# Kernel tuning notes

Hardware: AMD Instinct MI355X
Metric: run time of the kernel (lower is better)

The kernel has to match this reference:

```python
import jax, jax.numpy as jnp
import numpy as np

LAMBDA = 20.0
EPS = 1e-06
LAYER_WEIGHTS = (1.0, 0.5, 0.25, 0.125)


def _hungarian(cost):
    """Jonker-Volgenant shortest augmenting path LAP solver (same optimum as
    scipy.optimize.linear_sum_assignment). Returns col index per row."""
    cost = np.asarray(cost, dtype=np.float64)
    n = cost.shape[0]
    INF = 1e18
    u = np.zeros(n + 1)
    v = np.zeros(n + 1)
    p = np.zeros(n + 1, dtype=np.int64)   # p[j] = row matched to col j (1-indexed)
    way = np.zeros(n + 1, dtype=np.int64)
    for i in range(1, n + 1):
        p[0] = i
        j0 = 0
        minv = np.full(n + 1, INF)
        used = np.zeros(n + 1, dtype=bool)
        while True:
            used[j0] = True
            i0 = p[j0]
            free = np.nonzero(~used[1:])[0] + 1  # unused cols (1-indexed)
            cur = cost[i0 - 1, free - 1] - u[i0] - v[free]
            better = cur < minv[free]
            minv[free] = np.where(better, cur, minv[free])
            way[free] = np.where(better, j0, way[free])
            k = free[np.argmin(minv[free])]
            delta = minv[k]
            u[p[used]] += delta
            v[np.nonzero(used)[0]] -= delta
            minv[~used] -= delta
            j0 = k
            if p[j0] == 0:
                break
        while j0:
            j1 = way[j0]
            p[j0] = p[j1]
            j0 = j1
    col_of_row = np.zeros(n, dtype=np.int32)
    for j in range(1, n + 1):
        col_of_row[p[j] - 1] = j - 1
    return col_of_row


def _lap_cols(cost):
    n = cost.shape[0]
    return jax.pure_callback(
        lambda c: _hungarian(np.asarray(c)),
        jax.ShapeDtypeStruct((n,), np.int32),
        cost)


def _one_hot_matching(cols, n):
    return jnp.zeros((n, n), dtype=jnp.float32).at[jnp.arange(n), cols].set(1.0)


def _lap_solve_impl(cost):
    n = cost.shape[0]
    return _one_hot_matching(_lap_cols(cost), n)


@jax.custom_vjp
def lap_solve(cost):
    return _lap_solve_impl(cost)


def _lap_fwd(cost):
    lab = _lap_solve_impl(cost)
    return lab, (cost, lab)


def _lap_bwd(res, g):
    # Blackbox differentiation (Vlastelica et al.): re-solve on perturbed costs.
    cost, lab = res
    lab_bwd = _lap_solve_impl(cost + LAMBDA * g)
    return (-(lab - lab_bwd) / (LAMBDA + EPS),)


lap_solve.defvjp(_lap_fwd, _lap_bwd)


def _mse_dist(A, B):
    # [N, d] x [N, d] -> [N, N] mean-squared-error matrix
    d = A.shape[1]
    sq = jnp.sum(A * A, axis=1)[:, None] - 2.0 * (A @ B.T) + jnp.sum(B * B, axis=1)[None, :]
    return jnp.clip(sq, 0.0) / d


def _hamming(pred, ideal):
    err = pred * (1.0 - ideal) + (1.0 - pred) * ideal
    return err.mean(axis=0).sum()


def setup_inputs() -> dict:
    key = jax.random.key(0)
    ks = jax.random.split(key, 6)
    N = 384
    dims = (16384, 16384, 8192, 8192)
    inp = {}
    for i, d in enumerate(dims):
        inp[f"latent{i}"] = jax.random.normal(ks[i], (2, N, d), dtype=jnp.float32)
    inp["inv_perm_A"] = jax.random.permutation(ks[4], N).astype(jnp.int64)
    inp["inv_perm_B"] = jax.random.permutation(ks[5], N).astype(jnp.int64)
    return inp


def reference(latent0, latent1, latent2, latent3, inv_perm_A, inv_perm_B):
    latents = (latent0, latent1, latent2, latent3)
    N = latent0.shape[1]
    ideal = jnp.zeros((N, N), dtype=jnp.float32).at[inv_perm_A, inv_perm_B].set(1.0)
    combined = jnp.zeros((N, N), dtype=jnp.float32)
    total = jnp.float32(0.0)
    for w, lat in zip(LAYER_WEIGHTS, latents):
        A = lat[0].reshape(N, -1)
        B = lat[1].reshape(N, -1)
        cost = _mse_dist(A, B)
        combined = combined + w * cost
        pred = lap_solve(cost)
        total = total + w * _hamming(pred, ideal)
    final = lap_solve(combined)
    col_ind = jnp.argmax(final, axis=1).astype(jnp.int32)
    row_ind = jnp.arange(N, dtype=jnp.int32)
    return total, row_ind, col_ind
```

## Files before the change

kernel.cpp:

```cpp
#include <hip/hip_runtime.h>

#define NN 384
#define ARR_CAP 1000
#define MARKV 0x7FFFFFFF
#define BIG0  0x7FFFFFF0
#define SATK  ((1 << 28) - 1)

#define SETV6(a, k, val) do{ switch(k){ \
  case 0: a[0]=(val); break; case 1: a[1]=(val); break; case 2: a[2]=(val); break; \
  case 3: a[3]=(val); break; case 4: a[4]=(val); break; default: a[5]=(val); } }while(0)

__device__ __forceinline__ void lds_fence() {
  asm volatile("s_waitcnt lgkmcnt(0)" ::: "memory");
}

__device__ __forceinline__ int sel6b(const int (&a)[6], int k) {
  int x01 = (k & 1) ? a[1] : a[0];
  int x23 = (k & 1) ? a[3] : a[2];
  int x45 = (k & 1) ? a[5] : a[4];
  int xlo = (k & 2) ? x23 : x01;
  return (k & 4) ? x45 : xlo;
}

template<int CTRL>
__device__ __forceinline__ int dpp_i32(int x) {
  return __builtin_amdgcn_update_dpp(0x7FFFFFFF, x, CTRL, 0xF, 0xF, false);
}

__device__ __forceinline__ int wave_min_i32(int m) {
#define ST(C) { int o = dpp_i32<C>(m); m = min(m, o); }
  ST(0xB1) ST(0x4E) ST(0x124) ST(0x128) ST(0x142) ST(0x143)
#undef ST
  return __builtin_amdgcn_readlane(m, 63);
}

__device__ __forceinline__ void wave_min2_i32(int& m1, int& m2) {
#define ST(C) { int o1 = dpp_i32<C>(m1); int o2 = dpp_i32<C>(m2); \
                int hi = max(m1, o1); m1 = min(m1, o1); m2 = min(min(m2, o2), hi); }
  ST(0xB1) ST(0x4E) ST(0x124) ST(0x128) ST(0x142) ST(0x143)
#undef ST
  m1 = __builtin_amdgcn_readlane(m1, 63);
  m2 = __builtin_amdgcn_readlane(m2, 63);
}

__global__ __launch_bounds__(256) void row_norms_k(const float* __restrict__ x0,
                                                   const float* __restrict__ x1,
                                                   const float* __restrict__ x2,
                                                   const float* __restrict__ x3,
                                                   float* __restrict__ out,
                                                   int K0, int K1, int K2, int K3) {
  int layer = blockIdx.y;
  const float* X = layer == 0 ? x0 : layer == 1 ? x1 : layer == 2 ? x2 : x3;
  int K = layer == 0 ? K0 : layer == 1 ? K1 : layer == 2 ? K2 : K3;
  int row = blockIdx.x;
  int tid = threadIdx.x;
  const float4* xp = (const float4*)(X + (size_t)row * K);
  int K4 = K >> 2;
  float s = 0.f;
  for (int k = tid; k < K4; k += 256) {
    float4 x = xp[k];
    s = fmaf(x.x, x.x, s); s = fmaf(x.y, x.y, s);
    s = fmaf(x.z, x.z, s); s = fmaf(x.w, x.w, s);
  }
  __shared__ float red[256];
  red[tid] = s;
  __syncthreads();
  for (int st = 128; st > 0; st >>= 1) {
    if (tid < st) red[tid] += red[tid + st];
    __syncthreads();
  }
  if (tid == 0) out[layer * 768 + row] = red[0];
}

__global__ __launch_bounds__(256) void gemm_partial_k(const float* __restrict__ A,
                                                      const float* __restrict__ B,
                                                      float* __restrict__ pbuf,
                                                      int K, int kslice, int S) {
  __shared__ float As[16][64];
  __shared__ float Bs[16][64];
  const int tid = threadIdx.x;
  const int row0 = blockIdx.y * 64;
  const int col0 = blockIdx.x * 64;
  const int sz = blockIdx.z;
  const int tm = (tid >> 4) << 2;
  const int tn = (tid & 15) << 2;
  const int lr = tid >> 2;
  const int lk = (tid & 3) << 2;
  const float* ap = A + (size_t)(row0 + lr) * K + (size_t)sz * kslice + lk;
  const float* bp = B + (size_t)(col0 + lr) * K + (size_t)sz * kslice + lk;
  float acc[4][4] = {};
  for (int k0 = 0; k0 < kslice; k0 += 16) {
    float4 av = *(const float4*)(ap + k0);
    float4 bv = *(const float4*)(bp + k0);
    __syncthreads();
    As[lk + 0][lr] = av.x; As[lk + 1][lr] = av.y; As[lk + 2][lr] = av.z; As[lk + 3][lr] = av.w;
    Bs[lk + 0][lr] = bv.x; Bs[lk + 1][lr] = bv.y; Bs[lk + 2][lr] = bv.z; Bs[lk + 3][lr] = bv.w;
    __syncthreads();
    float t[4][4] = {};
#pragma unroll
    for (int kk = 0; kk < 16; ++kk) {
      float4 a = *(const float4*)&As[kk][tm];
      float4 b = *(const float4*)&Bs[kk][tn];
      t[0][0] = fmaf(a.x, b.x, t[0][0]); t[0][1] = fmaf(a.x, b.y, t[0][1]);
      t[0][2] = fmaf(a.x, b.z, t[0][2]); t[0][3] = fmaf(a.x, b.w, t[0][3]);
      t[1][0] = fmaf(a.y, b.x, t[1][0]); t[1][1] = fmaf(a.y, b.y, t[1][1]);
      t[1][2] = fmaf(a.y, b.z, t[1][2]); t[1][3] = fmaf(a.y, b.w, t[1][3]);
      t[2][0] = fmaf(a.z, b.x, t[2][0]); t[2][1] = fmaf(a.z, b.y, t[2][1]);
      t[2][2] = fmaf(a.z, b.z, t[2][2]); t[2][3] = fmaf(a.z, b.w, t[2][3]);
      t[3][0] = fmaf(a.w, b.x, t[3][0]); t[3][1] = fmaf(a.w, b.y, t[3][1]);
      t[3][2] = fmaf(a.w, b.z, t[3][2]); t[3][3] = fmaf(a.w, b.w, t[3][3]);
    }
#pragma unroll
    for (int m = 0; m < 4; ++m)
#pragma unroll
      for (int n = 0; n < 4; ++n) acc[m][n] += t[m][n];
  }
  float* pb = pbuf + (((size_t)(blockIdx.y * 6 + blockIdx.x) * S + sz) << 12);
#pragma unroll
  for (int m = 0; m < 4; ++m)
#pragma unroll
    for (int n = 0; n < 4; ++n)
      pb[((tm + m) << 6) | (tn + n)] = acc[m][n];
}

__global__ __launch_bounds__(256) void cost_finalize_k(const float* __restrict__ pbuf,
                                                       const float* __restrict__ sa,
                                                       const float* __restrict__ sb,
                                                       float* __restrict__ C,
                                                       int S, float inv_ds) {
  int idx = blockIdx.x * 256 + threadIdx.x;
  if (idx >= NN * NN) return;
  int i = idx / NN;
  int j = idx - i * NN;
  int t = (i >> 6) * 6 + (j >> 6);
  int w = ((i & 63) << 6) | (j & 63);
  const float* p = pbuf + ((size_t)t * S << 12) + w;
  float dot = 0.f;
  for (int s = 0; s < S; ++s) dot += p[(size_t)s << 12];
  float sq = (sa[i] - 2.0f * dot) + sb[j];
  C[idx] = fmaxf(sq, 0.0f) * inv_ds;
}

__global__ __launch_bounds__(256) void gemm_cost_k(const float* __restrict__ A,
                                                   const float* __restrict__ B,
                                                   const float* __restrict__ sa,
                                                   const float* __restrict__ sb,
                                                   float* __restrict__ C,
                                                   int K, float inv_ds) {
  __shared__ float As[16][64];
  __shared__ float Bs[16][64];
  const int tid = threadIdx.x;
  const int row0 = blockIdx.y * 64;
  const int col0 = blockIdx.x * 64;
  const int tm = (tid >> 4) << 2;
  const int tn = (tid & 15) << 2;
  const int lr = tid >> 2;
  const int lk = (tid & 3) << 2;
  const float* ap = A + (size_t)(row0 + lr) * K + lk;
  const float* bp = B + (size_t)(col0 + lr) * K + lk;
  float acc[4][4] = {};
  for (int k0 = 0; k0 < K; k0 += 16) {
    float4 av = *(const float4*)(ap + k0);
    float4 bv = *(const float4*)(bp + k0);
    __syncthreads();
    As[lk + 0][lr] = av.x; As[lk + 1][lr] = av.y; As[lk + 2][lr] = av.z; As[lk + 3][lr] = av.w;
    Bs[lk + 0][lr] = bv.x; Bs[lk + 1][lr] = bv.y; Bs[lk + 2][lr] = bv.z; Bs[lk + 3][lr] = bv.w;
    __syncthreads();
#pragma unroll
    for (int kk = 0; kk < 16; ++kk) {
      float4 a = *(const float4*)&As[kk][tm];
      float4 b = *(const float4*)&Bs[kk][tn];
      acc[0][0] = fmaf(a.x, b.x, acc[0][0]); acc[0][1] = fmaf(a.x, b.y, acc[0][1]);
      acc[0][2] = fmaf(a.x, b.z, acc[0][2]); acc[0][3] = fmaf(a.x, b.w, acc[0][3]);
      acc[1][0] = fmaf(a.y, b.x, acc[1][0]); acc[1][1] = fmaf(a.y, b.y, acc[1][1]);
      acc[1][2] = fmaf(a.y, b.z, acc[1][2]); acc[1][3] = fmaf(a.y, b.w, acc[1][3]);
      acc[2][0] = fmaf(a.z, b.x, acc[2][0]); acc[2][1] = fmaf(a.z, b.y, acc[2][1]);
      acc[2][2] = fmaf(a.z, b.z, acc[2][2]); acc[2][3] = fmaf(a.z, b.w, acc[2][3]);
      acc[3][0] = fmaf(a.w, b.x, acc[3][0]); acc[3][1] = fmaf(a.w, b.y, acc[3][1]);
      acc[3][2] = fmaf(a.w, b.z, acc[3][2]); acc[3][3] = fmaf(a.w, b.w, acc[3][3]);
    }
  }
#pragma unroll
  for (int m = 0; m < 4; ++m) {
    int i = row0 + tm + m;
    float sai = sa[i];
#pragma unroll
    for (int n = 0; n < 4; ++n) {
      int j = col0 + tn + n;
      float sq = (sai - 2.0f * acc[m][n]) + sb[j];
      C[i * NN + j] = fmaxf(sq, 0.0f) * inv_ds;
    }
  }
}

__global__ __launch_bounds__(256) void combine_k(float* __restrict__ cost) {
  int idx = blockIdx.x * 256 + threadIdx.x;
  if (idx < NN * NN) {
    float c0 = cost[idx];
    float c1 = cost[1 * NN * NN + idx];
    float c2 = cost[2 * NN * NN + idx];
    float c3 = cost[3 * NN * NN + idx];
    float cc = c0 + 0.5f * c1 + 0.25f * c2 + 0.125f * c3;
    int* ci = (int*)cost;
    ci[idx] = (int)c0;
    ci[1 * NN * NN + idx] = (int)c1;
    ci[2 * NN * NN + idx] = (int)c2;
    ci[3 * NN * NN + idx] = (int)c3;
    ci[4 * NN * NN + idx] = (int)cc;
  }
}

__global__ __launch_bounds__(64) void lap_k(const int* __restrict__ costs,
                                            const long long* __restrict__ invA,
                                            const long long* __restrict__ invB,
                                            int* __restrict__ colofrow,
                                            int* __restrict__ mism) {
  const int prob = blockIdx.x;
  const int* __restrict__ Ci = costs + (size_t)prob * NN * NN;
  const int lane = threadIdx.x;

  __shared__ int u_si[NN];
  __shared__ int mrow_s[NN];
  __shared__ int rowpick_s[NN];
  __shared__ int rowfree_s[NN];
  __shared__ int q_s[512];
  __shared__ int list_s[NN];
  __shared__ int cofr_s[NN];
  __shared__ int ideal_s[NN];

  int vv[6];
  int mr[6];
  int umr[6];

  int vmin[6]; int imin[6];
#pragma unroll
  for (int k = 0; k < 6; ++k) { vmin[k] = 0x7FFFFFFF; imin[k] = 0; }
  {
    const int* p = Ci + lane;
#pragma unroll 4
    for (int i = 0; i < NN; ++i) {
#pragma unroll
      for (int k = 0; k < 6; ++k) {
        int c = p[(size_t)i * NN + (k << 6)];
        if (c < vmin[k]) { vmin[k] = c; imin[k] = i; }
      }
    }
  }
#pragma unroll
  for (int k = 0; k < 6; ++k) vv[k] = vmin[k];
#pragma unroll
  for (int k = 0; k < 6; ++k) {
    int r = lane + (k << 6);
    rowpick_s[r] = 0x7fffffff;
    rowfree_s[r] = 1;
    u_si[r] = 0;
  }
  for (int t = lane; t < 512; t += 64) q_s[t] = 0;
  lds_fence();
#pragma unroll
  for (int k = 0; k < 6; ++k) atomicMin(&rowpick_s[imin[k]], lane + (k << 6));
  lds_fence();
#pragma unroll
  for (int k = 0; k < 6; ++k) {
    int j = lane + (k << 6);
    int i1 = imin[k];
    int won = (rowpick_s[i1] == j);
    mrow_s[j] = won ? i1 : -1;
    mr[k] = won ? i1 : -1;
    if (won) rowfree_s[i1] = 0;
  }
  lds_fence();

  int mcount = 0;
#pragma unroll
  for (int k = 0; k < 6; ++k) {
    int r = lane + (k << 6);
    int mtc = (rowfree_s[r] == 0);
    unsigned long long msk = __ballot(mtc);
    if (mtc) list_s[mcount + (int)__popcll(msk & ((1ull << lane) - 1ull))] = r;
    mcount += (int)__popcll(msk);
  }
  int head = 0, tail = 0;
#pragma unroll
  for (int k = 0; k < 6; ++k) {
    int r = lane + (k << 6);
    int fr = rowfree_s[r];
    unsigned long long msk = __ballot(fr);
    if (fr) q_s[tail + (int)__popcll(msk & ((1ull << lane) - 1ull))] = r;
    tail += (int)__popcll(msk);
  }
  lds_fence();

  {
    int i_cur = 0;
    if (mcount > 0) i_cur = list_s[0];
    int cf[6];
#pragma unroll
    for (int k = 0; k < 6; ++k) cf[k] = Ci[(size_t)i_cur * NN + lane + (k << 6)];
    for (int idx = 0; idx < mcount; ++idx) {
      int i = i_cur;
      int cfc[6];
#pragma unroll
      for (int k = 0; k < 6; ++k) cfc[k] = cf[k];
      int inext = (idx + 1 < mcount) ? list_s[idx + 1] : i_cur;
      i_cur = inext;
#pragma unroll
      for (int k = 0; k < 6; ++k) cf[k] = Ci[(size_t)inext * NN + lane + (k << 6)];
      int j1 = rowpick_s[i];
      int kj = j1 >> 6, oj = j1 & 63;
      int m = 0x7FFFFFFF;
#pragma unroll
      for (int k = 0; k < 6; ++k) {
        int cur = cfc[k] - vv[k];
        bool excl = (k == kj) && (lane == oj);
        m = min(m, excl ? 0x7FFFFFFF : cur);
      }
      m = wave_min_i32(m);
      int cj1 = __builtin_amdgcn_readlane(sel6b(cfc, kj), oj);
      if (lane == oj) { SETV6(vv, kj, cj1 - m); }
      if (lane == 0) u_si[i] = m;
    }
  }
  lds_fence();

  {
    int pre_for = -1, i_pre = 0;
    int cf[6];
#pragma unroll
    for (int k = 0; k < 6; ++k) cf[k] = 0;
    if (head < tail) {
      i_pre = q_s[head & 511];
      pre_for = head;
#pragma unroll
      for (int k = 0; k < 6; ++k) cf[k] = Ci[(size_t)i_pre * NN + lane + (k << 6)];
    }
    for (int it = 0; it < ARR_CAP && head < tail; ++it) {
      int i;
      int cfc[6];
      if (pre_for == head) {
        i = i_pre;
#pragma unroll
        for (int k = 0; k < 6; ++k) cfc[k] = cf[k];
      } else {
        i = q_s[head & 511];
#pragma unroll
        for (int k = 0; k < 6; ++k) cfc[k] = Ci[(size_t)i * NN + lane + (k << 6)];
      }
      head++;
      int nxt = q_s[head & 511];
      bool pvalid = (head < tail);
      i_pre = nxt;
      pre_for = pvalid ? head : -1;
#pragma unroll
      for (int k = 0; k < 6; ++k) cf[k] = Ci[(size_t)i_pre * NN + lane + (k << 6)];

      int pk[6];
#pragma unroll
      for (int k = 0; k < 6; ++k) {
        int cur = cfc[k] - vv[k];
        int key = min(cur, SATK);
        pk[k] = (key << 3) | k;
      }
      int l1 = min(pk[0], pk[1]), h1 = max(pk[0], pk[1]);
      int l2 = min(pk[2], pk[3]), h2 = max(pk[2], pk[3]);
      int l3 = min(pk[4], pk[5]), h3 = max(pk[4], pk[5]);
      int lm1 = min(min(l1, l2), l3);
      int med = max(min(l1, l2), min(max(l1, l2), l3));
      int lm2 = min(med, min(min(h1, h2), h3));
      int m1 = lm1, m2 = lm2;
      wave_min2_i32(m1, m2);
      unsigned long long bm = __ballot(lm1 == m1);
      int src = (int)__builtin_ctzll(bm);
      int kj = m1 & 7;
      int j1 = src + (kj << 6);
      int u1 = m1 >> 3, u2 = m2 >> 3;
      int i0 = __builtin_amdgcn_readlane(sel6b(mr, kj), src);
      bool tiebad = (u1 == u2) && (i0 >= 0);
      if (!tiebad) {
        if (u1 < u2) {
          if (lane == src) { SETV6(vv, kj, vv[kj] - (u2 - u1)); }
        }
        if (lane == src) { SETV6(mr, kj, i); }
        if (lane == 0) {
          mrow_s[j1] = i;
          rowfree_s[i] = 0;
          u_si[i] = u2;
          if (i0 >= 0) { rowfree_s[i0] = 1; q_s[tail & 511] = i0; }
        }
        if (i0 >= 0) tail++;
      }
      lds_fence();
    }
  }

#pragma unroll
  for (int k = 0; k < 6; ++k) {
    int r = mr[k];
    umr[k] = (r < 0) ? 0 : u_si[max(r, 0)];
  }
  int ntodo = 0;
#pragma unroll
  for (int k = 0; k < 6; ++k) {
    int r = lane + (k << 6);
    int fr = rowfree_s[r];
    unsigned long long msk = __ballot(fr);
    if (fr) q_s[ntodo + (int)__popcll(msk & ((1ull << lane) - 1ull))] = r;
    ntodo += (int)__popcll(msk);
  }
  lds_fence();

  for (int fi = 0; fi < ntodo; ++fi) {
    int f = q_s[fi];
    int minv[6], dj[6], wy[6];
#pragma unroll
    for (int k = 0; k < 6; ++k) { minv[k] = BIG0; dj[k] = 0; wy[k] = -1; }
    int D = 0, markj = -1, j1 = -1, j2p = -1;
    int specv = 0;
    int ui0 = u_si[f];
    const int uif = ui0;
    int cs[6], sp[6];
#pragma unroll
    for (int k = 0; k < 6; ++k) sp[k] = 0;
    {
      const int* crow0 = Ci + (size_t)f * NN;
#pragma unroll
      for (int k = 0; k < 6; ++k) cs[k] = crow0[lane + (k << 6)];
    }
    for (;;) {
      int s = ui0 - D;
      int pk[6];
#pragma unroll
      for (int k = 0; k < 6; ++k) {
        int cur = (cs[k] - s) - vv[k];
        bool domark = ((lane + (k << 6)) == markj);
        bool used = (minv[k] == MARKV);
        bool upd = (cur < minv[k]) && !used && !domark;
        minv[k] = domark ? MARKV : (upd ? cur : minv[k]);
        dj[k] = domark ? D : dj[k];
        wy[k] = upd ? markj : wy[k];
        int diff = minv[k] - D;
        int key = min(diff, SATK);
        pk[k] = (key << 3) | k;
      }
      int l1 = min(pk[0], pk[1]), h1 = max(pk[0], pk[1]);
      int l2 = min(pk[2], pk[3]), h2 = max(pk[2], pk[3]);
      int l3 = min(pk[4], pk[5]), h3 = max(pk[4], pk[5]);
      int lm1 = min(min(l1, l2), l3);
      int med = max(min(l1, l2), min(max(l1, l2), l3));
      int lm2 = min(med, min(min(h1, h2), h3));
      int m1 = wave_min_i32(lm1);
      unsigned long long bm = __ballot(lm1 == m1);
      int src = (int)__builtin_ctzll(bm);
      int kj = m1 & 7;
      j1 = src + (kj << 6);
      D += (m1 >> 3);
      int r = __builtin_amdgcn_readlane(sel6b(mr, kj), src);
      int ur = __builtin_amdgcn_readlane(sel6b(umr, kj), src);
      if (r < 0) break;
      bool hit = specv && (j1 == j2p);
      if (hit) {
#pragma unroll
        for (int k = 0; k < 6; ++k) cs[k] = sp[k];
      } else {
        const int* crow = Ci + (size_t)r * NN;
#pragma unroll
        for (int k = 0; k < 6; ++k) cs[k] = crow[lane + (k << 6)];
      }
      {
        int cand = (lane == src) ? lm2 : lm1;
        int m2 = wave_min_i32(cand);
        unsigned long long bm2 = __ballot(cand == m2);
        int src2 = (int)__builtin_ctzll(bm2 | 1ull);
        int kj2 = m2 & 7;
        int j2 = src2 + (kj2 << 6);
        int r2 = __builtin_amdgcn_readlane(sel6b(mr, kj2), src2);
        bool j2ok = ((m2 >> 3) < SATK);
        bool dospec = j2ok && (r2 >= 0) && (j2 != j1);
        if (dospec) {
          const int* crow2 = Ci + (size_t)r2 * NN;
#pragma unroll
          for (int k = 0; k < 6; ++k) sp[k] = crow2[lane + (k << 6)];
        }
        specv = dospec; j2p = j2;
      }
      markj = j1; ui0 = ur;
    }
#pragma unroll
    for (int k = 0; k < 6; ++k) {
      if (minv[k] == MARKV) {
        int upd = D - dj[k];
        vv[k] -= upd;
        u_si[mr[k]] += upd;
      }
    }
    if (lane == 0) u_si[f] = uif + D;
    {
      int j = j1, jprev = -1;
      for (;;) {
        int kjw = j >> 6, ojw = j & 63;
        int jp = __builtin_amdgcn_readlane(sel6b(wy, kjw), ojw);
        int rc = __builtin_amdgcn_readlane(sel6b(mr, kjw), ojw);
        if (jprev >= 0 && lane == 0) mrow_s[jprev] = rc;
        if (jp < 0) { if (lane == 0) mrow_s[j] = f; break; }
        jprev = j; j = jp;
      }
    }
    lds_fence();
#pragma unroll
    for (int k = 0; k < 6; ++k) mr[k] = mrow_s[lane + (k << 6)];
#pragma unroll
    for (int k = 0; k < 6; ++k) {
      int rr = mr[k];
      umr[k] = (rr < 0) ? 0 : u_si[max(rr, 0)];
    }
  }

  lds_fence();
#pragma unroll
  for (int k = 0; k < 6; ++k) {
    int j = lane + (k << 6);
    cofr_s[mrow_s[j]] = j;
    ideal_s[(int)invA[j]] = (int)invB[j];
  }
  lds_fence();
  int cnt = 0;
#pragma unroll
  for (int k = 0; k < 6; ++k) {
    int r = lane + (k << 6);
    colofrow[prob * NN + r] = cofr_s[r];
    cnt += (cofr_s[r] != ideal_s[r]) ? 1 : 0;
  }
#pragma unroll
  for (int off = 1; off < 64; off <<= 1) cnt += __shfl_xor(cnt, off, 64);
  if (lane == 0 && prob < 4) mism[prob] = cnt;
}

__global__ __launch_bounds__(384) void finalize_k(const int* __restrict__ colofrow,
                                                  const int* __restrict__ mism,
                                                  float* __restrict__ out) {
  int t = threadIdx.x;
  if (t == 0) {
    const double w[4] = {1.0, 0.5, 0.25, 0.125};
    double tot = 0.0;
    for (int l = 0; l < 4; ++l) tot += w[l] * (2.0 * (double)mism[l] / (double)NN);
    out[0] = (float)tot;
  }
  out[1 + t] = (float)t;
  out[1 + NN + t] = (float)colofrow[4 * NN + t];
}

extern "C" void kernel_launch(void* const* d_in, const int* in_sizes, int n_in,
                              void* d_out, int out_size, void* d_ws, size_t ws_size,
                              hipStream_t stream) {
  const float* lat[4] = {(const float*)d_in[0], (const float*)d_in[1],
                         (const float*)d_in[2], (const float*)d_in[3]};
  const long long* invA = (const long long*)d_in[4];
  const long long* invB = (const long long*)d_in[5];

  float* ws = (float*)d_ws;
  float* cost = ws;
  float* norms = ws + 5 * NN * NN;
  int* colofrow = (int*)(norms + 4 * 768);
  int* mism = colofrow + 5 * NN;
  float* pbuf = (float*)(mism + 8);

  int K[4];
  for (int l = 0; l < 4; ++l) K[l] = in_sizes[l] / (2 * NN);

  size_t base = (size_t)(5 * NN * NN + 4 * 768 + 5 * NN + 8);
  int S = 0;
  for (int cand = 32; cand >= 8; cand >>= 1) {
    if (ws_size >= (base + (size_t)36 * cand * 4096) * 4) { S = cand; break; }
  }

  row_norms_k<<<dim3(768, 4), 256, 0, stream>>>(
      lat[0], lat[1], lat[2], lat[3], norms, K[0], K[1], K[2], K[3]);

  if (S > 0) {
    for (int l = 0; l < 4; ++l) {
      float inv_ds = 16777216.0f / (float)K[l];
      gemm_partial_k<<<dim3(6, 6, S), 256, 0, stream>>>(
          lat[l], lat[l] + (size_t)NN * K[l], pbuf, K[l], K[l] / S, S);
      cost_finalize_k<<<(NN * NN + 255) / 256, 256, 0, stream>>>(
          pbuf, norms + l * 768, norms + l * 768 + NN,
          cost + (size_t)l * NN * NN, S, inv_ds);
    }
  } else {
    for (int l = 0; l < 4; ++l) {
      float inv_ds = 16777216.0f / (float)K[l];
      gemm_cost_k<<<dim3(6, 6), 256, 0, stream>>>(
          lat[l], lat[l] + (size_t)NN * K[l], norms + l * 768, norms + l * 768 + NN,
          cost + (size_t)l * NN * NN, K[l], inv_ds);
    }
  }
  combine_k<<<(NN * NN + 255) / 256, 256, 0, stream>>>(cost);
  lap_k<<<5, 64, 0, stream>>>((const int*)cost, invA, invB, colofrow, mism);
  finalize_k<<<1, NN, 0, stream>>>(colofrow, mism, (float*)d_out);
}
```

Before: 3.421 ms.

## Double-buffer speculative row prefetch and prefetch next free row in LAP solver

The augmenting-path loop now keeps two speculative prefetched cost rows (A/B slots with tags) instead of one. This raises the chance that the next selected column's row is already in registers and avoids a dependent global load. The next free row's costs are prefetched before the dual update of the current augmentation, and the auction phase skips useless prefetches and refills the prefetch slot when a displaced row is enqueued. The change also raises ARR_CAP and the unroll of the column-min loop, which costs more registers and risks lower occupancy or spills.

```diff
diff --git a/kernel.cpp b/kernel.cpp
--- a/kernel.cpp
+++ b/kernel.cpp
@@ -1,7 +1,7 @@
 #include <hip/hip_runtime.h>
 
 #define NN 384
-#define ARR_CAP 1000
+#define ARR_CAP 1200
 #define MARKV 0x7FFFFFFF
 #define BIG0  0x7FFFFFF0
 #define SATK  ((1 << 28) - 1)
@@ -237,7 +237,7 @@
   for (int k = 0; k < 6; ++k) { vmin[k] = 0x7FFFFFFF; imin[k] = 0; }
   {
     const int* p = Ci + lane;
-#pragma unroll 4
+#pragma unroll 8
     for (int i = 0; i < NN; ++i) {
 #pragma unroll
       for (int k = 0; k < 6; ++k) {
@@ -351,8 +351,10 @@
       bool pvalid = (head < tail);
       i_pre = nxt;
       pre_for = pvalid ? head : -1;
-#pragma unroll
-      for (int k = 0; k < 6; ++k) cf[k] = Ci[(size_t)i_pre * NN + lane + (k << 6)];
+      if (pvalid) {
+#pragma unroll
+        for (int k = 0; k < 6; ++k) cf[k] = Ci[(size_t)i_pre * NN + lane + (k << 6)];
+      }
 
       int pk[6];
 #pragma unroll
@@ -388,6 +390,11 @@
           if (i0 >= 0) { rowfree_s[i0] = 1; q_s[tail & 511] = i0; }
         }
         if (i0 >= 0) tail++;
+        if (pre_for < 0 && i0 >= 0) {
+          i_pre = i0; pre_for = head;
+#pragma unroll
+          for (int k = 0; k < 6; ++k) cf[k] = Ci[(size_t)i0 * NN + lane + (k << 6)];
+        }
       }
       lds_fence();
     }
@@ -409,23 +416,27 @@
   }
   lds_fence();
 
+  int csp[6];
+  if (ntodo > 0) {
+    int f0 = q_s[0];
+    const int* crow0 = Ci + (size_t)f0 * NN;
+#pragma unroll
+    for (int k = 0; k < 6; ++k) csp[k] = crow0[lane + (k << 6)];
+  }
+
   for (int fi = 0; fi < ntodo; ++fi) {
     int f = q_s[fi];
     int minv[6], dj[6], wy[6];
 #pragma unroll
     for (int k = 0; k < 6; ++k) { minv[k] = BIG0; dj[k] = 0; wy[k] = -1; }
-    int D = 0, markj = -1, j1 = -1, j2p = -1;
-    int specv = 0;
+    int D = 0, markj = -1, j1 = -1;
+    int tagA = -1, tagB = -1;
+    bool aNewer = false;
     int ui0 = u_si[f];
     const int uif = ui0;
-    int cs[6], sp[6];
-#pragma unroll
-    for (int k = 0; k < 6; ++k) sp[k] = 0;
-    {
-      const int* crow0 = Ci + (size_t)f * NN;
-#pragma unroll
-      for (int k = 0; k < 6; ++k) cs[k] = crow0[lane + (k << 6)];
-    }
+    int cs[6], spA[6], spB[6];
+#pragma unroll
+    for (int k = 0; k < 6; ++k) { cs[k] = csp[k]; spA[k] = 0; spB[k] = 0; }
     for (;;) {
       int s = ui0 - D;
       int pk[6];
@@ -457,10 +468,15 @@
       int r = __builtin_amdgcn_readlane(sel6b(mr, kj), src);
       int ur = __builtin_amdgcn_readlane(sel6b(umr, kj), src);
       if (r < 0) break;
-      bool hit = specv && (j1 == j2p);
-      if (hit) {
-#pragma unroll
-        for (int k = 0; k < 6; ++k) cs[k] = sp[k];
+      bool hitA = (j1 == tagA), hitB = (j1 == tagB);
+      if (hitA) {
+#pragma unroll
+        for (int k = 0; k < 6; ++k) cs[k] = spA[k];
+        aNewer = false;
+      } else if (hitB) {
+#pragma unroll
+        for (int k = 0; k < 6; ++k) cs[k] = spB[k];
+        aNewer = true;
       } else {
         const int* crow = Ci + (size_t)r * NN;
 #pragma unroll
@@ -469,21 +485,33 @@
       {
         int cand = (lane == src) ? lm2 : lm1;
         int m2 = wave_min_i32(cand);
-        unsigned long long bm2 = __ballot(cand == m2);
-        int src2 = (int)__builtin_ctzll(bm2 | 1ull);
-        int kj2 = m2 & 7;
-        int j2 = src2 + (kj2 << 6);
-        int r2 = __builtin_amdgcn_readlane(sel6b(mr, kj2), src2);
-        bool j2ok = ((m2 >> 3) < SATK);
-        bool dospec = j2ok && (r2 >= 0) && (j2 != j1);
-        if (dospec) {
-          const int* crow2 = Ci + (size_t)r2 * NN;
-#pragma unroll
-          for (int k = 0; k < 6; ++k) sp[k] = crow2[lane + (k << 6)];
+        if ((m2 >> 3) < SATK) {
+          unsigned long long bm2 = __ballot(cand == m2);
+          int src2 = (int)__builtin_ctzll(bm2 | 1ull);
+          int kj2 = m2 & 7;
+          int j2 = src2 + (kj2 << 6);
+          int r2 = __builtin_amdgcn_readlane(sel6b(mr, kj2), src2);
+          if (r2 >= 0 && j2 != j1 && j2 != tagA && j2 != tagB) {
+            const int* crow2 = Ci + (size_t)r2 * NN;
+            if (!aNewer) {
+#pragma unroll
+              for (int k = 0; k < 6; ++k) spA[k] = crow2[lane + (k << 6)];
+              tagA = j2; aNewer = true;
+            } else {
+#pragma unroll
+              for (int k = 0; k < 6; ++k) spB[k] = crow2[lane + (k << 6)];
+              tagB = j2; aNewer = false;
+            }
+          }
         }
-        specv = dospec; j2p = j2;
       }
       markj = j1; ui0 = ur;
+    }
+    if (fi + 1 < ntodo) {
+      int fn = q_s[fi + 1];
+      const int* crown = Ci + (size_t)fn * NN;
+#pragma unroll
+      for (int k = 0; k < 6; ++k) csp[k] = crown[lane + (k << 6)];
     }
 #pragma unroll
     for (int k = 0; k < 6; ++k) {
```

Result: slower. 3.496 ms (+2.2%).
